# Kernel optimization log

Measured on AMD Instinct MI355X. Metric: run time of the kernel, lower is better.

Reference implementation:

```python
import jax, jax.numpy as jnp
import numpy as np

N_NODES = 50000
IN, H, OUT = 128, 256, 128  # in_channels, hidden_channels, out_channels
E, PE = 640000, 500000
EPS = 1e-5


def setup_inputs() -> dict:
    key = jax.random.key(0)
    ks = jax.random.split(key, 12)
    def rn(k, shape, s=0.05):
        return jax.random.normal(k, shape, jnp.float32) * s
    return {
        "x": jax.random.normal(ks[0], (N_NODES, IN), jnp.float32),
        "edge_index": jax.random.randint(ks[1], (2, E), 0, N_NODES, jnp.int32),
        "pred_edge_index": jax.random.randint(ks[2], (2, PE), 0, N_NODES, jnp.int32),
        # SAGEConv 1: out = mean_neighbors @ W_l^T + x @ W_r^T + b (PyG default, root_weight=True)
        "W1l": rn(ks[3], (H, IN)), "W1r": rn(ks[4], (H, IN)), "b1": jnp.zeros((H,), jnp.float32),
        "bn1_g": jnp.ones((H,), jnp.float32), "bn1_b": jnp.zeros((H,), jnp.float32),
        "bn1_m": jnp.zeros((H,), jnp.float32), "bn1_v": jnp.ones((H,), jnp.float32),
        # SAGEConv 2
        "W2l": rn(ks[5], (OUT, H)), "W2r": rn(ks[6], (OUT, H)), "b2": jnp.zeros((OUT,), jnp.float32),
        # LinkPredictor MLP
        "pW1": rn(ks[7], (H, 2 * OUT)), "pb1": jnp.zeros((H,), jnp.float32),
        "pbn1_g": jnp.ones((H,), jnp.float32), "pbn1_b": jnp.zeros((H,), jnp.float32),
        "pbn1_m": jnp.zeros((H,), jnp.float32), "pbn1_v": jnp.ones((H,), jnp.float32),
        "pW2": rn(ks[8], (H // 2, H)), "pb2": jnp.zeros((H // 2,), jnp.float32),
        "pbn2_g": jnp.ones((H // 2,), jnp.float32), "pbn2_b": jnp.zeros((H // 2,), jnp.float32),
        "pbn2_m": jnp.zeros((H // 2,), jnp.float32), "pbn2_v": jnp.ones((H // 2,), jnp.float32),
        "pW3": rn(ks[9], (1, H // 2)), "pb3": jnp.zeros((1,), jnp.float32),
    }


def _bn(x, g, b, m, v):
    # BatchNorm1d in eval mode (running stats)
    return (x - m) * jax.lax.rsqrt(v + EPS) * g + b


def _sage(x, src, dst, Wl, Wr, b):
    # mean aggregation of source features onto targets (gather-scatter)
    agg = jax.ops.segment_sum(x[src], dst, num_segments=N_NODES)
    cnt = jax.ops.segment_sum(jnp.ones(src.shape, x.dtype), dst, num_segments=N_NODES)
    mean = agg / jnp.maximum(cnt, 1.0)[:, None]
    return mean @ Wl.T + x @ Wr.T + b


def reference(x, edge_index, pred_edge_index, W1l, W1r, b1, bn1_g, bn1_b, bn1_m, bn1_v,
              W2l, W2r, b2, pW1, pb1, pbn1_g, pbn1_b, pbn1_m, pbn1_v,
              pW2, pb2, pbn2_g, pbn2_b, pbn2_m, pbn2_v, pW3, pb3):
    src, dst = edge_index[0], edge_index[1]
    # encoder (dropout is identity in eval mode)
    h = _sage(x, src, dst, W1l, W1r, b1)
    h = jax.nn.relu(_bn(h, bn1_g, bn1_b, bn1_m, bn1_v))
    z = _sage(h, src, dst, W2l, W2r, b2)  # [N_NODES, OUT]
    # decoder: gather endpoint embeddings and run MLP
    q = jnp.concatenate([z[pred_edge_index[0]], z[pred_edge_index[1]]], axis=-1)  # [PE, 2*OUT]
    q = jax.nn.relu(_bn(q @ pW1.T + pb1, pbn1_g, pbn1_b, pbn1_m, pbn1_v))
    q = jax.nn.relu(_bn(q @ pW2.T + pb2, pbn2_g, pbn2_b, pbn2_m, pbn2_v))
    return (q @ pW3.T + pb3).squeeze(-1)  # [PE]
```

## Files before the change

### kernel.cpp

```cpp
#include <hip/hip_runtime.h>
#include <hip/hip_bf16.h>

#define NN   50000
#define NE   640000
#define NPE  500000
#define FEPS 1e-5f

typedef __attribute__((ext_vector_type(8))) short          bf16x8;
typedef __attribute__((ext_vector_type(8))) unsigned short u16x8;
typedef __attribute__((ext_vector_type(4))) float          f32x4;

__device__ inline float b2f(unsigned short u) {
    union { unsigned int i; float f; } c; c.i = (unsigned int)u << 16; return c.f;
}
__device__ inline unsigned short f2b(float f) {
    __hip_bfloat16 h = __float2bfloat16(f);
    return *reinterpret_cast<unsigned short*>(&h);
}

__global__ __launch_bounds__(256) void k_init(
    int4* __restrict__ zdst,
    const float* __restrict__ x, unsigned short* __restrict__ xbf,
    const float* __restrict__ W1l, const float* __restrict__ W1r,
    const float* __restrict__ W2l, const float* __restrict__ W2r,
    const float* __restrict__ pW1, const float* __restrict__ pW2,
    unsigned short* __restrict__ wdst) {
    int b = blockIdx.x, t = threadIdx.x;
    if (b < 196) {
        int i = b * 256 + t;
        if (i < 50048) zdst[i] = make_int4(0, 0, 0, 0);
        return;
    }
    const float* src;
    size_t off;
    if (b < 3321) {
        int i = (b - 196) * 256 + t;
        if (i >= 800000) return;
        const float4* p = (const float4*)x + 2 * (size_t)i;
        float4 a = p[0], c = p[1];
        u16x8 o;
        o[0]=f2b(a.x); o[1]=f2b(a.y); o[2]=f2b(a.z); o[3]=f2b(a.w);
        o[4]=f2b(c.x); o[5]=f2b(c.y); o[6]=f2b(c.z); o[7]=f2b(c.w);
        *((u16x8*)xbf + i) = o;
        return;
    }
    int i = (b - 3321) * 256 + t;
    if (i >= 28672) return;
    if      (i < 4096)  { src = W1l; off = i; }
    else if (i < 8192)  { src = W1r; off = i - 4096; }
    else if (i < 12288) { src = W2l; off = i - 8192; }
    else if (i < 16384) { src = W2r; off = i - 12288; }
    else if (i < 24576) { src = pW1; off = i - 16384; }
    else                { src = pW2; off = i - 24576; }
    const float4* p = (const float4*)src + 2 * off;
    float4 a = p[0], c = p[1];
    u16x8 o;
    o[0]=f2b(a.x); o[1]=f2b(a.y); o[2]=f2b(a.z); o[3]=f2b(a.w);
    o[4]=f2b(c.x); o[5]=f2b(c.y); o[6]=f2b(c.z); o[7]=f2b(c.w);
    *((u16x8*)wdst + i) = o;
}

__global__ void k_hist(const int* __restrict__ key, int* __restrict__ cnt, int n) {
    int e = blockIdx.x * blockDim.x + threadIdx.x;
    if (e < n) atomicAdd(&cnt[key[e]], 1);
}

__global__ void k_scan1(const int* __restrict__ cnt, int* __restrict__ part) {
    int t = threadIdx.x, lane = t & 63, w = t >> 6;
    int i = blockIdx.x * 256 + t;
    int v = (i < NN) ? cnt[i] : 0;
#pragma unroll
    for (int d = 1; d < 64; d <<= 1) v += __shfl_xor(v, d, 64);
    __shared__ int ws[4];
    if (lane == 0) ws[w] = v;
    __syncthreads();
    if (t == 0) part[blockIdx.x] = ws[0] + ws[1] + ws[2] + ws[3];
}

__global__ void k_scan2(int* __restrict__ part) {
    int t = threadIdx.x, lane = t & 63, w = t >> 6;
    int v = (t < 196) ? part[t] : 0;
    int s = v;
#pragma unroll
    for (int d = 1; d < 64; d <<= 1) { int u = __shfl_up(s, d, 64); if (lane >= d) s += u; }
    __shared__ int ws[4];
    if (lane == 63) ws[w] = s;
    __syncthreads();
    if (t == 0) { int a = 0; for (int k = 0; k < 4; ++k) { int tmp = ws[k]; ws[k] = a; a += tmp; } }
    __syncthreads();
    if (t < 196) part[t] = ws[w] + s - v;
}

__global__ void k_scan3(const int* __restrict__ cnt, const int* __restrict__ part,
                        int* __restrict__ rowptr) {
    int t = threadIdx.x, lane = t & 63, w = t >> 6;
    int i = blockIdx.x * 256 + t;
    int v = (i < NN) ? cnt[i] : 0;
    int s = v;
#pragma unroll
    for (int d = 1; d < 64; d <<= 1) { int u = __shfl_up(s, d, 64); if (lane >= d) s += u; }
    __shared__ int ws[4];
    if (lane == 63) ws[w] = s;
    __syncthreads();
    if (t == 0) { int a = 0; for (int k = 0; k < 4; ++k) { int tmp = ws[k]; ws[k] = a; a += tmp; } }
    __syncthreads();
    if (i <= NN) rowptr[i] = part[blockIdx.x] + ws[w] + s - v;
}

__global__ void k_fill(const int* __restrict__ src, const int* __restrict__ dst,
                       const int* __restrict__ rowptr, int* __restrict__ cursor,
                       int* __restrict__ col) {
    int e = blockIdx.x * blockDim.x + threadIdx.x;
    if (e >= NE) return;
    int d = dst[e];
    int slot = atomicAdd(&cursor[d], 1);
    col[rowptr[d] + slot] = src[e];
}

__global__ void k_fill2(const int* __restrict__ pu, const int* __restrict__ pv,
                        const int* __restrict__ rowptr2, int* __restrict__ cursor2,
                        int* __restrict__ su, int2* __restrict__ svi) {
    int e = blockIdx.x * blockDim.x + threadIdx.x;
    if (e >= NPE) return;
    int u = pu[e];
    int slot = atomicAdd(&cursor2[u], 1);
    int pos = rowptr2[u] + slot;
    su[pos] = u;
    svi[pos] = make_int2(pv[e], e);
}

__global__ __launch_bounds__(256) void k_mean(const unsigned short* __restrict__ feat,
                                              const int* __restrict__ rowptr,
                                              const int* __restrict__ col,
                                              unsigned short* __restrict__ outm) {
    int node = blockIdx.x * 4 + (threadIdx.x >> 6);
    int lane = threadIdx.x & 63;
    if (node >= NN) return;
    int beg = rowptr[node], end = rowptr[node + 1];
    float a0 = 0.f, a1 = 0.f;
    int j = beg;
    for (; j + 8 <= end; j += 8) {
        int s[8];
#pragma unroll
        for (int k = 0; k < 8; ++k) s[k] = col[j + k];
        unsigned int v[8];
#pragma unroll
        for (int k = 0; k < 8; ++k)
            v[k] = *(const unsigned int*)(feat + (size_t)s[k] * 128 + lane * 2);
#pragma unroll
        for (int k = 0; k < 8; ++k) { a0 += b2f(v[k] & 0xffff); a1 += b2f(v[k] >> 16); }
    }
    if (j + 4 <= end) {
        int s[4];
#pragma unroll
        for (int k = 0; k < 4; ++k) s[k] = col[j + k];
        unsigned int v[4];
#pragma unroll
        for (int k = 0; k < 4; ++k)
            v[k] = *(const unsigned int*)(feat + (size_t)s[k] * 128 + lane * 2);
#pragma unroll
        for (int k = 0; k < 4; ++k) { a0 += b2f(v[k] & 0xffff); a1 += b2f(v[k] >> 16); }
        j += 4;
    }
    for (; j < end; ++j) {
        int s = col[j];
        unsigned int v = *(const unsigned int*)(feat + (size_t)s * 128 + lane * 2);
        a0 += b2f(v & 0xffff); a1 += b2f(v >> 16);
    }
    float inv = 1.f / fmaxf((float)(end - beg), 1.f);
    unsigned int v = (unsigned int)f2b(a0 * inv) | ((unsigned int)f2b(a1 * inv) << 16);
    *(unsigned int*)(outm + (size_t)node * 128 + lane * 2) = v;
}

__global__ __launch_bounds__(256) void k_sage12(
    const unsigned short* __restrict__ mean, const unsigned short* __restrict__ self,
    const unsigned short* __restrict__ Wl, const unsigned short* __restrict__ Wr,
    const float* __restrict__ b, const float* __restrict__ bg, const float* __restrict__ bb,
    const float* __restrict__ bm, const float* __restrict__ bv,
    const unsigned short* __restrict__ W2l, const unsigned short* __restrict__ W2r,
    const float* __restrict__ b2,
    unsigned short* __restrict__ Y, unsigned short* __restrict__ S) {
    __shared__ unsigned short AB[64 * 256];
    unsigned short* ms = AB;
    unsigned short* xs = AB + 64 * 128;
    int t = threadIdx.x;
    int n0 = blockIdx.x * 64;
    for (int j = 0; j < 4; ++j) {
        int idx = t + j * 256;
        int row = idx >> 4, c16 = idx & 15;
        int node = n0 + row;
        u16x8 v = {0,0,0,0,0,0,0,0}, v2 = {0,0,0,0,0,0,0,0};
        if (node < NN) {
            v  = *(const u16x8*)(mean + (size_t)node * 128 + c16 * 8);
            v2 = *(const u16x8*)(self + (size_t)node * 128 + c16 * 8);
        }
        int byte = row * 256 + ((c16 * 16) ^ ((row & 7) << 4));
        *(u16x8*)((char*)ms + byte) = v;
        *(u16x8*)((char*)xs + byte) = v2;
    }
    __syncthreads();
    int w = t >> 6, l = t & 63, lr = l & 15, lh = l >> 4;
    f32x4 acc[4][4];
#pragma unroll
    for (int mi = 0; mi < 4; ++mi)
#pragma unroll
        for (int ni = 0; ni < 4; ++ni) { acc[mi][ni][0]=0; acc[mi][ni][1]=0; acc[mi][ni][2]=0; acc[mi][ni][3]=0; }
#pragma unroll
    for (int half = 0; half < 2; ++half) {
        const unsigned short* A = half ? xs : ms;
        const unsigned short* W = half ? Wr : Wl;
#pragma unroll
        for (int ks = 0; ks < 4; ++ks) {
            int k0 = ks * 32;
            bf16x8 a[4], wf[4];
#pragma unroll
            for (int mi = 0; mi < 4; ++mi) {
                int row = mi * 16 + lr;
                int byte = row * 256 + ((k0 * 2 + lh * 16) ^ ((row & 7) << 4));
                a[mi] = *(const bf16x8*)((const char*)A + byte);
            }
#pragma unroll
            for (int ni = 0; ni < 4; ++ni) {
                int wrow = w * 64 + ni * 16 + lr;
                wf[ni] = *(const bf16x8*)(W + (size_t)wrow * 128 + k0 + lh * 8);
            }
#pragma unroll
            for (int mi = 0; mi < 4; ++mi)
#pragma unroll
                for (int ni = 0; ni < 4; ++ni)
                    acc[mi][ni] = __builtin_amdgcn_mfma_f32_16x16x32_bf16(a[mi], wf[ni], acc[mi][ni], 0, 0, 0);
        }
    }
    __syncthreads();
#pragma unroll
    for (int ni = 0; ni < 4; ++ni) {
        int ch = w * 64 + ni * 16 + lr;
        float sc = bg[ch] * rsqrtf(bv[ch] + FEPS);
        float sh = bb[ch] - bm[ch] * sc;
        float bias = b[ch];
#pragma unroll
        for (int mi = 0; mi < 4; ++mi)
#pragma unroll
            for (int r = 0; r < 4; ++r) {
                int row = mi * 16 + lh * 4 + r;
                float vv = fmaxf((acc[mi][ni][r] + bias) * sc + sh, 0.f);
                int byte = row * 512 + ((ch * 2) ^ ((row & 7) << 4));
                *(unsigned short*)((char*)AB + byte) = f2b(vv);
            }
    }
    __syncthreads();
    f32x4 aY[4][2], aS[4][2];
#pragma unroll
    for (int mi = 0; mi < 4; ++mi)
#pragma unroll
        for (int ni = 0; ni < 2; ++ni) {
            aY[mi][ni][0]=0; aY[mi][ni][1]=0; aY[mi][ni][2]=0; aY[mi][ni][3]=0;
            aS[mi][ni][0]=0; aS[mi][ni][1]=0; aS[mi][ni][2]=0; aS[mi][ni][3]=0;
        }
#pragma unroll
    for (int ks = 0; ks < 8; ++ks) {
        int k0 = ks * 32;
        bf16x8 a[4], wl[2], wr[2];
#pragma unroll
        for (int mi = 0; mi < 4; ++mi) {
            int row = mi * 16 + lr;
            int byte = row * 512 + ((k0 * 2 + lh * 16) ^ ((row & 7) << 4));
            a[mi] = *(const bf16x8*)((const char*)AB + byte);
        }
#pragma unroll
        for (int ni = 0; ni < 2; ++ni) {
            int wrow = w * 32 + ni * 16 + lr;
            wl[ni] = *(const bf16x8*)(W2l + (size_t)wrow * 256 + k0 + lh * 8);
            wr[ni] = *(const bf16x8*)(W2r + (size_t)wrow * 256 + k0 + lh * 8);
        }
#pragma unroll
        for (int mi = 0; mi < 4; ++mi)
#pragma unroll
            for (int ni = 0; ni < 2; ++ni) {
                aY[mi][ni] = __builtin_amdgcn_mfma_f32_16x16x32_bf16(a[mi], wl[ni], aY[mi][ni], 0, 0, 0);
                aS[mi][ni] = __builtin_amdgcn_mfma_f32_16x16x32_bf16(a[mi], wr[ni], aS[mi][ni], 0, 0, 0);
            }
    }
#pragma unroll
    for (int ni = 0; ni < 2; ++ni) {
        int ch = w * 32 + ni * 16 + lr;
        float bias = b2[ch];
#pragma unroll
        for (int mi = 0; mi < 4; ++mi)
#pragma unroll
            for (int r = 0; r < 4; ++r) {
                int node = n0 + mi * 16 + lh * 4 + r;
                if (node < NN) {
                    Y[(size_t)node * 128 + ch] = f2b(aY[mi][ni][r]);
                    S[(size_t)node * 128 + ch] = f2b(aS[mi][ni][r] + bias);
                }
            }
    }
}

__global__ __launch_bounds__(256) void k_prep(
    const unsigned short* __restrict__ S,
    const unsigned short* __restrict__ mY,
    const unsigned short* __restrict__ W1,
    const float* __restrict__ b1, const float* __restrict__ g1,
    const float* __restrict__ be1, const float* __restrict__ m1, const float* __restrict__ v1,
    unsigned short* __restrict__ Pa, unsigned short* __restrict__ Pb) {
    __shared__ unsigned short zs[64 * 128];
    int t = threadIdx.x;
    int tile = blockIdx.x >> 1, side = blockIdx.x & 1;
    int n0 = tile * 64;
    for (int j = 0; j < 4; ++j) {
        int idx = t + j * 256;
        int row = idx >> 4, c16 = idx & 15;
        int node = n0 + row;
        u16x8 o = {0,0,0,0,0,0,0,0};
        if (node < NN) {
            u16x8 sv = *(const u16x8*)(S  + (size_t)node * 128 + c16 * 8);
            u16x8 mv = *(const u16x8*)(mY + (size_t)node * 128 + c16 * 8);
#pragma unroll
            for (int jj = 0; jj < 8; ++jj)
                o[jj] = f2b(b2f((unsigned short)sv[jj]) + b2f((unsigned short)mv[jj]));
        }
        int byte = row * 256 + ((c16 * 16) ^ ((row & 7) << 4));
        *(u16x8*)((char*)zs + byte) = o;
    }
    __syncthreads();
    int w = t >> 6, l = t & 63, lr = l & 15, lh = l >> 4;
    f32x4 acc[4][4];
#pragma unroll
    for (int mi = 0; mi < 4; ++mi)
#pragma unroll
        for (int ni = 0; ni < 4; ++ni) { acc[mi][ni][0]=0; acc[mi][ni][1]=0; acc[mi][ni][2]=0; acc[mi][ni][3]=0; }
#pragma unroll
    for (int ks = 0; ks < 4; ++ks) {
        int k0 = ks * 32;
        bf16x8 a[4], wf[4];
#pragma unroll
        for (int mi = 0; mi < 4; ++mi) {
            int row = mi * 16 + lr;
            int byte = row * 256 + ((k0 * 2 + lh * 16) ^ ((row & 7) << 4));
            a[mi] = *(const bf16x8*)((const char*)zs + byte);
        }
#pragma unroll
        for (int ni = 0; ni < 4; ++ni) {
            int ch = w * 64 + ni * 16 + lr;
            wf[ni] = *(const bf16x8*)(W1 + (size_t)ch * 256 + side * 128 + k0 + lh * 8);
        }
#pragma unroll
        for (int mi = 0; mi < 4; ++mi)
#pragma unroll
            for (int ni = 0; ni < 4; ++ni)
                acc[mi][ni] = __builtin_amdgcn_mfma_f32_16x16x32_bf16(a[mi], wf[ni], acc[mi][ni], 0, 0, 0);
    }
    unsigned short* P = side ? Pb : Pa;
#pragma unroll
    for (int ni = 0; ni < 4; ++ni) {
        int ch = w * 64 + ni * 16 + lr;
        float sc = g1[ch] * rsqrtf(v1[ch] + FEPS);
        float add = side ? 0.f : ((b1[ch] - m1[ch]) * sc + be1[ch]);
#pragma unroll
        for (int mi = 0; mi < 4; ++mi)
#pragma unroll
            for (int r = 0; r < 4; ++r) {
                int node = n0 + mi * 16 + lh * 4 + r;
                if (node < NN)
                    P[(size_t)node * 256 + ch] = f2b(acc[mi][ni][r] * sc + add);
            }
    }
}

__global__ __launch_bounds__(256, 5) void k_mlp(
    const unsigned short* __restrict__ Pa, const unsigned short* __restrict__ Pb,
    const int* __restrict__ su, const int2* __restrict__ svi,
    const unsigned short* __restrict__ W2, const float* __restrict__ b2,
    const float* __restrict__ g2, const float* __restrict__ be2,
    const float* __restrict__ m2, const float* __restrict__ v2,
    const float* __restrict__ W3, const float* __restrict__ b3,
    float* __restrict__ out) {
    __shared__ unsigned short q1[64 * 256];
    int t = threadIdx.x;
    const int q = 976, r = 5;
    int bid = blockIdx.x;
    int xcd = bid & 7, ii = bid >> 3;
    int wg = (xcd < r) ? (xcd * (q + 1) + ii) : (r * (q + 1) + (xcd - r) * q + ii);
    int e0 = wg * 64;
#pragma unroll
    for (int batch = 0; batch < 2; ++batch) {
        u16x8 A[4], B[4];
        int bofs[4];
#pragma unroll
        for (int j = 0; j < 4; ++j) {
            int idx = t + (batch * 4 + j) * 256;
            int edge = idx >> 5, c16 = idx & 31;
            int ge = e0 + edge;
            if (ge < NPE) {
                int u = su[ge];
                int2 vi = svi[ge];
                A[j] = *(const u16x8*)(Pa + (size_t)u    * 256 + c16 * 8);
                B[j] = *(const u16x8*)(Pb + (size_t)vi.x * 256 + c16 * 8);
            } else {
                A[j] = (u16x8){0,0,0,0,0,0,0,0};
                B[j] = (u16x8){0,0,0,0,0,0,0,0};
            }
            bofs[j] = edge * 512 + ((c16 * 16) ^ ((edge & 7) << 4));
        }
#pragma unroll
        for (int j = 0; j < 4; ++j) {
            u16x8 o;
#pragma unroll
            for (int jj = 0; jj < 8; ++jj)
                o[jj] = f2b(fmaxf(b2f((unsigned short)A[j][jj]) + b2f((unsigned short)B[j][jj]), 0.f));
            *(u16x8*)((char*)q1 + bofs[j]) = o;
        }
    }
    __syncthreads();
    int w = t >> 6, l = t & 63, lr = l & 15, lh = l >> 4;
    f32x4 acc[4][2];
#pragma unroll
    for (int mi = 0; mi < 4; ++mi)
#pragma unroll
        for (int ni = 0; ni < 2; ++ni) { acc[mi][ni][0]=0; acc[mi][ni][1]=0; acc[mi][ni][2]=0; acc[mi][ni][3]=0; }
#pragma unroll
    for (int ks = 0; ks < 8; ++ks) {
        int k0 = ks * 32;
        bf16x8 a[4], wf[2];
#pragma unroll
        for (int mi = 0; mi < 4; ++mi) {
            int row = mi * 16 + lr;
            int byte = row * 512 + ((k0 * 2 + lh * 16) ^ ((row & 7) << 4));
            a[mi] = *(const bf16x8*)((const char*)q1 + byte);
        }
#pragma unroll
        for (int ni = 0; ni < 2; ++ni) {
            int wrow = w * 32 + ni * 16 + lr;
            wf[ni] = *(const bf16x8*)(W2 + (size_t)wrow * 256 + k0 + lh * 8);
        }
#pragma unroll
        for (int mi = 0; mi < 4; ++mi)
#pragma unroll
            for (int ni = 0; ni < 2; ++ni)
                acc[mi][ni] = __builtin_amdgcn_mfma_f32_16x16x32_bf16(a[mi], wf[ni], acc[mi][ni], 0, 0, 0);
    }
    __syncthreads();
#pragma unroll
    for (int ni = 0; ni < 2; ++ni) {
        int ch = w * 32 + ni * 16 + lr;
        float sc = g2[ch] * rsqrtf(v2[ch] + FEPS);
        float sh = be2[ch] - m2[ch] * sc;
        float bias = b2[ch];
#pragma unroll
        for (int mi = 0; mi < 4; ++mi)
#pragma unroll
            for (int r = 0; r < 4; ++r) {
                int row = mi * 16 + lh * 4 + r;
                float vv = fmaxf((acc[mi][ni][r] + bias) * sc + sh, 0.f);
                int byte = row * 256 + ((ch * 2) ^ ((row & 7) << 4));
                *(unsigned short*)((char*)q1 + byte) = f2b(vv);
            }
    }
    __syncthreads();
    {
        int edge = t >> 2, part = t & 3;
        float p = 0.f;
#pragma unroll
        for (int s = 0; s < 4; ++s) {
            int byte = edge * 256 + ((part * 64 + s * 16) ^ ((edge & 7) << 4));
            u16x8 v = *(const u16x8*)((const char*)q1 + byte);
#pragma unroll
            for (int jj = 0; jj < 8; ++jj)
                p += b2f((unsigned short)v[jj]) * W3[part * 32 + s * 8 + jj];
        }
        p += __shfl_xor(p, 1, 64);
        p += __shfl_xor(p, 2, 64);
        int ge = e0 + edge;
        if (part == 0 && ge < NPE) out[svi[ge].y] = p + b3[0];
    }
}

extern "C" void kernel_launch(void* const* d_in, const int* in_sizes, int n_in,
                              void* d_out, int out_size, void* d_ws, size_t ws_size,
                              hipStream_t stream) {
    const float* x    = (const float*)d_in[0];
    const int*   ei   = (const int*)d_in[1];
    const int*   pei  = (const int*)d_in[2];
    const float* W1l  = (const float*)d_in[3];
    const float* W1r  = (const float*)d_in[4];
    const float* b1   = (const float*)d_in[5];
    const float* bn1g = (const float*)d_in[6];
    const float* bn1b = (const float*)d_in[7];
    const float* bn1m = (const float*)d_in[8];
    const float* bn1v = (const float*)d_in[9];
    const float* W2l  = (const float*)d_in[10];
    const float* W2r  = (const float*)d_in[11];
    const float* b2   = (const float*)d_in[12];
    const float* pW1  = (const float*)d_in[13];
    const float* pb1  = (const float*)d_in[14];
    const float* pg1  = (const float*)d_in[15];
    const float* pbb1 = (const float*)d_in[16];
    const float* pm1  = (const float*)d_in[17];
    const float* pv1  = (const float*)d_in[18];
    const float* pW2  = (const float*)d_in[19];
    const float* pb2  = (const float*)d_in[20];
    const float* pg2  = (const float*)d_in[21];
    const float* pbb2 = (const float*)d_in[22];
    const float* pm2  = (const float*)d_in[23];
    const float* pv2  = (const float*)d_in[24];
    const float* pW3  = (const float*)d_in[25];
    const float* pb3  = (const float*)d_in[26];
    float* out = (float*)d_out;

    const int* src = ei;
    const int* dst = ei + NE;
    const int* pu  = pei;
    const int* pv  = pei + NPE;

    char* p = (char*)d_ws;
    auto alloc = [&](size_t bytes) -> char* {
        char* r = p; p += (bytes + 255) & ~(size_t)255; return r;
    };
    int* cnt     = (int*)alloc((size_t)NN * 4);
    int* cursor  = (int*)alloc((size_t)NN * 4);
    int* cnt2    = (int*)alloc((size_t)NN * 4);
    int* cursor2 = (int*)alloc((size_t)NN * 4);
    int* part    = (int*)alloc(256 * 4);
    int* part2   = (int*)alloc(256 * 4);
    int* rowptr  = (int*)alloc((size_t)(NN + 1) * 4);
    int* rowptr2 = (int*)alloc((size_t)(NN + 1) * 4);
    int* col     = (int*)alloc((size_t)NE * 4);
    int* su      = (int*)alloc((size_t)NPE * 4);
    int2* svi    = (int2*)alloc((size_t)NPE * 8);
    unsigned short* xbf  = (unsigned short*)alloc((size_t)NN * 128 * 2);
    unsigned short* mx   = (unsigned short*)alloc((size_t)NN * 128 * 2);
    unsigned short* Ybf  = (unsigned short*)alloc((size_t)NN * 128 * 2);
    unsigned short* mY   = (unsigned short*)alloc((size_t)NN * 128 * 2);
    unsigned short* Sbf  = (unsigned short*)alloc((size_t)NN * 128 * 2);
    unsigned short* Pa   = (unsigned short*)alloc((size_t)NN * 256 * 2);
    unsigned short* W1lb = (unsigned short*)alloc((size_t)256 * 128 * 2);
    unsigned short* W1rb = (unsigned short*)alloc((size_t)256 * 128 * 2);
    unsigned short* W2lb = (unsigned short*)alloc((size_t)128 * 256 * 2);
    unsigned short* W2rb = (unsigned short*)alloc((size_t)128 * 256 * 2);
    unsigned short* pW1b = (unsigned short*)alloc((size_t)256 * 256 * 2);
    unsigned short* pW2b = (unsigned short*)alloc((size_t)128 * 256 * 2);
    unsigned short* Pb = xbf;

    k_init<<<3433, 256, 0, stream>>>((int4*)cnt, x, xbf,
                                     W1l, W1r, W2l, W2r, pW1, pW2, W1lb);
    k_hist<<<2500, 256, 0, stream>>>(dst, cnt, NE);
    k_scan1<<<196, 256, 0, stream>>>(cnt, part);
    k_scan2<<<1, 256, 0, stream>>>(part);
    k_scan3<<<196, 256, 0, stream>>>(cnt, part, rowptr);
    k_fill<<<2500, 256, 0, stream>>>(src, dst, rowptr, cursor, col);
    k_hist<<<1954, 256, 0, stream>>>(pu, cnt2, NPE);
    k_scan1<<<196, 256, 0, stream>>>(cnt2, part2);
    k_scan2<<<1, 256, 0, stream>>>(part2);
    k_scan3<<<196, 256, 0, stream>>>(cnt2, part2, rowptr2);
    k_fill2<<<1954, 256, 0, stream>>>(pu, pv, rowptr2, cursor2, su, svi);

    k_mean<<<12500, 256, 0, stream>>>(xbf, rowptr, col, mx);
    k_sage12<<<782, 256, 0, stream>>>(mx, xbf, W1lb, W1rb, b1, bn1g, bn1b, bn1m, bn1v,
                                      W2lb, W2rb, b2, Ybf, Sbf);
    k_mean<<<12500, 256, 0, stream>>>(Ybf, rowptr, col, mY);

    k_prep<<<1564, 256, 0, stream>>>(Sbf, mY, pW1b, pb1, pg1, pbb1, pm1, pv1, Pa, Pb);

    k_mlp<<<(NPE + 63) / 64, 256, 0, stream>>>(Pa, Pb, su, svi,
                                               pW2b, pb2, pg2, pbb2, pm2, pv2,
                                               pW3, pb3, out);
}
```

Before: 418.1 us.

## Drop prediction-edge sort and run MLP directly from registers without LDS

Removes the histogram, scan and fill passes that sorted prediction edges by source node, so the MLP kernel reads pu/pv directly and writes outputs in original order. The MLP kernel is restructured so each wave handles 16 edges, builds the MFMA A-operand straight from the gathered Pa+Pb rows in registers with software prefetch, and applies the folded BN2 scale and offset plus the W3 dot product with shuffles instead of staging through LDS. BN2 scale and offset are precomputed once in the init kernel. The cost is that gathers are no longer locality-sorted, and W2 is re-read per wave from global memory.

```diff
diff --git a/kernel.cpp b/kernel.cpp
--- a/kernel.cpp
+++ b/kernel.cpp
@@ -24,17 +24,28 @@
     const float* __restrict__ W1l, const float* __restrict__ W1r,
     const float* __restrict__ W2l, const float* __restrict__ W2r,
     const float* __restrict__ pW1, const float* __restrict__ pW2,
-    unsigned short* __restrict__ wdst) {
+    unsigned short* __restrict__ wdst,
+    const float* __restrict__ pb2, const float* __restrict__ pg2,
+    const float* __restrict__ pbb2, const float* __restrict__ pm2,
+    const float* __restrict__ pv2, float2* __restrict__ fold2) {
     int b = blockIdx.x, t = threadIdx.x;
-    if (b < 196) {
+    if (b < 98) {
         int i = b * 256 + t;
-        if (i < 50048) zdst[i] = make_int4(0, 0, 0, 0);
+        if (i < 25088) zdst[i] = make_int4(0, 0, 0, 0);
+        return;
+    }
+    if (b == 3335) {
+        if (t < 128) {
+            float sc = pg2[t] * rsqrtf(pv2[t] + FEPS);
+            float off = pb2[t] * sc + pbb2[t] - pm2[t] * sc;
+            fold2[t] = make_float2(sc, off);
+        }
         return;
     }
     const float* src;
     size_t off;
-    if (b < 3321) {
-        int i = (b - 196) * 256 + t;
+    if (b < 3223) {
+        int i = (b - 98) * 256 + t;
         if (i >= 800000) return;
         const float4* p = (const float4*)x + 2 * (size_t)i;
         float4 a = p[0], c = p[1];
@@ -44,7 +55,7 @@
         *((u16x8*)xbf + i) = o;
         return;
     }
-    int i = (b - 3321) * 256 + t;
+    int i = (b - 3223) * 256 + t;
     if (i >= 28672) return;
     if      (i < 4096)  { src = W1l; off = i; }
     else if (i < 8192)  { src = W1r; off = i - 4096; }
@@ -115,18 +126,6 @@
     int d = dst[e];
     int slot = atomicAdd(&cursor[d], 1);
     col[rowptr[d] + slot] = src[e];
-}
-
-__global__ void k_fill2(const int* __restrict__ pu, const int* __restrict__ pv,
-                        const int* __restrict__ rowptr2, int* __restrict__ cursor2,
-                        int* __restrict__ su, int2* __restrict__ svi) {
-    int e = blockIdx.x * blockDim.x + threadIdx.x;
-    if (e >= NPE) return;
-    int u = pu[e];
-    int slot = atomicAdd(&cursor2[u], 1);
-    int pos = rowptr2[u] + slot;
-    su[pos] = u;
-    svi[pos] = make_int2(pv[e], e);
 }
 
 __global__ __launch_bounds__(256) void k_mean(const unsigned short* __restrict__ feat,
@@ -371,109 +370,62 @@
 
 __global__ __launch_bounds__(256, 5) void k_mlp(
     const unsigned short* __restrict__ Pa, const unsigned short* __restrict__ Pb,
-    const int* __restrict__ su, const int2* __restrict__ svi,
-    const unsigned short* __restrict__ W2, const float* __restrict__ b2,
-    const float* __restrict__ g2, const float* __restrict__ be2,
-    const float* __restrict__ m2, const float* __restrict__ v2,
+    const int* __restrict__ pu, const int* __restrict__ pv,
+    const unsigned short* __restrict__ W2,
+    const float2* __restrict__ fold2,
     const float* __restrict__ W3, const float* __restrict__ b3,
     float* __restrict__ out) {
-    __shared__ unsigned short q1[64 * 256];
     int t = threadIdx.x;
-    const int q = 976, r = 5;
-    int bid = blockIdx.x;
-    int xcd = bid & 7, ii = bid >> 3;
-    int wg = (xcd < r) ? (xcd * (q + 1) + ii) : (r * (q + 1) + (xcd - r) * q + ii);
-    int e0 = wg * 64;
-#pragma unroll
-    for (int batch = 0; batch < 2; ++batch) {
-        u16x8 A[4], B[4];
-        int bofs[4];
-#pragma unroll
-        for (int j = 0; j < 4; ++j) {
-            int idx = t + (batch * 4 + j) * 256;
-            int edge = idx >> 5, c16 = idx & 31;
-            int ge = e0 + edge;
-            if (ge < NPE) {
-                int u = su[ge];
-                int2 vi = svi[ge];
-                A[j] = *(const u16x8*)(Pa + (size_t)u    * 256 + c16 * 8);
-                B[j] = *(const u16x8*)(Pb + (size_t)vi.x * 256 + c16 * 8);
-            } else {
-                A[j] = (u16x8){0,0,0,0,0,0,0,0};
-                B[j] = (u16x8){0,0,0,0,0,0,0,0};
-            }
-            bofs[j] = edge * 512 + ((c16 * 16) ^ ((edge & 7) << 4));
-        }
-#pragma unroll
-        for (int j = 0; j < 4; ++j) {
-            u16x8 o;
-#pragma unroll
-            for (int jj = 0; jj < 8; ++jj)
-                o[jj] = f2b(fmaxf(b2f((unsigned short)A[j][jj]) + b2f((unsigned short)B[j][jj]), 0.f));
-            *(u16x8*)((char*)q1 + bofs[j]) = o;
-        }
-    }
-    __syncthreads();
     int w = t >> 6, l = t & 63, lr = l & 15, lh = l >> 4;
-    f32x4 acc[4][2];
-#pragma unroll
-    for (int mi = 0; mi < 4; ++mi)
-#pragma unroll
-        for (int ni = 0; ni < 2; ++ni) { acc[mi][ni][0]=0; acc[mi][ni][1]=0; acc[mi][ni][2]=0; acc[mi][ni][3]=0; }
+    int we0 = blockIdx.x * 64 + w * 16;
+    int eidx = we0 + lr;
+    int u = 0, v = 0;
+    if (eidx < NPE) { u = pu[eidx]; v = pv[eidx]; }
+    const u16x8* rowA = (const u16x8*)(Pa + (size_t)u * 256 + lh * 8);
+    const u16x8* rowB = (const u16x8*)(Pb + (size_t)v * 256 + lh * 8);
+    f32x4 acc[8];
+#pragma unroll
+    for (int ni = 0; ni < 8; ++ni) { acc[ni][0]=0; acc[ni][1]=0; acc[ni][2]=0; acc[ni][3]=0; }
+    u16x8 pa0 = rowA[0], pb0 = rowB[0];
+    u16x8 pa1 = rowA[4], pb1 = rowB[4];
 #pragma unroll
     for (int ks = 0; ks < 8; ++ks) {
-        int k0 = ks * 32;
-        bf16x8 a[4], wf[2];
-#pragma unroll
-        for (int mi = 0; mi < 4; ++mi) {
-            int row = mi * 16 + lr;
-            int byte = row * 512 + ((k0 * 2 + lh * 16) ^ ((row & 7) << 4));
-            a[mi] = *(const bf16x8*)((const char*)q1 + byte);
-        }
-#pragma unroll
-        for (int ni = 0; ni < 2; ++ni) {
-            int wrow = w * 32 + ni * 16 + lr;
-            wf[ni] = *(const bf16x8*)(W2 + (size_t)wrow * 256 + k0 + lh * 8);
-        }
-#pragma unroll
-        for (int mi = 0; mi < 4; ++mi)
-#pragma unroll
-            for (int ni = 0; ni < 2; ++ni)
-                acc[mi][ni] = __builtin_amdgcn_mfma_f32_16x16x32_bf16(a[mi], wf[ni], acc[mi][ni], 0, 0, 0);
-    }
-    __syncthreads();
-#pragma unroll
-    for (int ni = 0; ni < 2; ++ni) {
-        int ch = w * 32 + ni * 16 + lr;
-        float sc = g2[ch] * rsqrtf(v2[ch] + FEPS);
-        float sh = be2[ch] - m2[ch] * sc;
-        float bias = b2[ch];
-#pragma unroll
-        for (int mi = 0; mi < 4; ++mi)
-#pragma unroll
-            for (int r = 0; r < 4; ++r) {
-                int row = mi * 16 + lh * 4 + r;
-                float vv = fmaxf((acc[mi][ni][r] + bias) * sc + sh, 0.f);
-                int byte = row * 256 + ((ch * 2) ^ ((row & 7) << 4));
-                *(unsigned short*)((char*)q1 + byte) = f2b(vv);
-            }
-    }
-    __syncthreads();
-    {
-        int edge = t >> 2, part = t & 3;
-        float p = 0.f;
-#pragma unroll
-        for (int s = 0; s < 4; ++s) {
-            int byte = edge * 256 + ((part * 64 + s * 16) ^ ((edge & 7) << 4));
-            u16x8 v = *(const u16x8*)((const char*)q1 + byte);
-#pragma unroll
-            for (int jj = 0; jj < 8; ++jj)
-                p += b2f((unsigned short)v[jj]) * W3[part * 32 + s * 8 + jj];
-        }
-        p += __shfl_xor(p, 1, 64);
-        p += __shfl_xor(p, 2, 64);
-        int ge = e0 + edge;
-        if (part == 0 && ge < NPE) out[svi[ge].y] = p + b3[0];
+        bf16x8 af;
+#pragma unroll
+        for (int jj = 0; jj < 8; ++jj) {
+            float f = fmaxf(b2f((unsigned short)pa0[jj]) + b2f((unsigned short)pb0[jj]), 0.f);
+            af[jj] = (short)f2b(f);
+        }
+        pa0 = pa1; pb0 = pb1;
+        if (ks < 6) { pa1 = rowA[(ks + 2) * 4]; pb1 = rowB[(ks + 2) * 4]; }
+#pragma unroll
+        for (int ni = 0; ni < 8; ++ni) {
+            bf16x8 wf = *(const bf16x8*)(W2 + (size_t)(ni * 16 + lr) * 256 + ks * 32 + lh * 8);
+            acc[ni] = __builtin_amdgcn_mfma_f32_16x16x32_bf16(af, wf, acc[ni], 0, 0, 0);
+        }
+    }
+    float p0 = 0.f, p1 = 0.f, p2 = 0.f, p3 = 0.f;
+#pragma unroll
+    for (int ni = 0; ni < 8; ++ni) {
+        int ch = ni * 16 + lr;
+        float2 f = fold2[ch];
+        float w3 = W3[ch];
+        p0 += fmaxf(acc[ni][0] * f.x + f.y, 0.f) * w3;
+        p1 += fmaxf(acc[ni][1] * f.x + f.y, 0.f) * w3;
+        p2 += fmaxf(acc[ni][2] * f.x + f.y, 0.f) * w3;
+        p3 += fmaxf(acc[ni][3] * f.x + f.y, 0.f) * w3;
+    }
+#pragma unroll
+    for (int d = 1; d < 16; d <<= 1) {
+        p0 += __shfl_xor(p0, d, 16);
+        p1 += __shfl_xor(p1, d, 16);
+        p2 += __shfl_xor(p2, d, 16);
+        p3 += __shfl_xor(p3, d, 16);
+    }
+    if (lr < 4) {
+        int oe = we0 + lh * 4 + lr;
+        float pr = (lr == 0) ? p0 : (lr == 1) ? p1 : (lr == 2) ? p2 : p3;
+        if (oe < NPE) out[oe] = pr + b3[0];
     }
 }
 
@@ -520,15 +472,9 @@
     };
     int* cnt     = (int*)alloc((size_t)NN * 4);
     int* cursor  = (int*)alloc((size_t)NN * 4);
-    int* cnt2    = (int*)alloc((size_t)NN * 4);
-    int* cursor2 = (int*)alloc((size_t)NN * 4);
     int* part    = (int*)alloc(256 * 4);
-    int* part2   = (int*)alloc(256 * 4);
     int* rowptr  = (int*)alloc((size_t)(NN + 1) * 4);
-    int* rowptr2 = (int*)alloc((size_t)(NN + 1) * 4);
     int* col     = (int*)alloc((size_t)NE * 4);
-    int* su      = (int*)alloc((size_t)NPE * 4);
-    int2* svi    = (int2*)alloc((size_t)NPE * 8);
     unsigned short* xbf  = (unsigned short*)alloc((size_t)NN * 128 * 2);
     unsigned short* mx   = (unsigned short*)alloc((size_t)NN * 128 * 2);
     unsigned short* Ybf  = (unsigned short*)alloc((size_t)NN * 128 * 2);
@@ -541,20 +487,17 @@
     unsigned short* W2rb = (unsigned short*)alloc((size_t)128 * 256 * 2);
     unsigned short* pW1b = (unsigned short*)alloc((size_t)256 * 256 * 2);
     unsigned short* pW2b = (unsigned short*)alloc((size_t)128 * 256 * 2);
+    float2* fold2        = (float2*)alloc(128 * 8);
     unsigned short* Pb = xbf;
 
-    k_init<<<3433, 256, 0, stream>>>((int4*)cnt, x, xbf,
-                                     W1l, W1r, W2l, W2r, pW1, pW2, W1lb);
+    k_init<<<3336, 256, 0, stream>>>((int4*)cnt, x, xbf,
+                                     W1l, W1r, W2l, W2r, pW1, pW2, W1lb,
+                                     pb2, pg2, pbb2, pm2, pv2, fold2);
     k_hist<<<2500, 256, 0, stream>>>(dst, cnt, NE);
     k_scan1<<<196, 256, 0, stream>>>(cnt, part);
     k_scan2<<<1, 256, 0, stream>>>(part);
     k_scan3<<<196, 256, 0, stream>>>(cnt, part, rowptr);
     k_fill<<<2500, 256, 0, stream>>>(src, dst, rowptr, cursor, col);
-    k_hist<<<1954, 256, 0, stream>>>(pu, cnt2, NPE);
-    k_scan1<<<196, 256, 0, stream>>>(cnt2, part2);
-    k_scan2<<<1, 256, 0, stream>>>(part2);
-    k_scan3<<<196, 256, 0, stream>>>(cnt2, part2, rowptr2);
-    k_fill2<<<1954, 256, 0, stream>>>(pu, pv, rowptr2, cursor2, su, svi);
 
     k_mean<<<12500, 256, 0, stream>>>(xbf, rowptr, col, mx);
     k_sage12<<<782, 256, 0, stream>>>(mx, xbf, W1lb, W1rb, b1, bn1g, bn1b, bn1m, bn1v,
@@ -563,7 +506,6 @@
 
     k_prep<<<1564, 256, 0, stream>>>(Sbf, mY, pW1b, pb1, pg1, pbb1, pm1, pv1, Pa, Pb);
 
-    k_mlp<<<(NPE + 63) / 64, 256, 0, stream>>>(Pa, Pb, su, svi,
-                                               pW2b, pb2, pg2, pbb2, pm2, pv2,
-                                               pW3, pb3, out);
-}
+    k_mlp<<<(NPE + 63) / 64, 256, 0, stream>>>(Pa, Pb, pu, pv,
+                                               pW2b, fold2, pW3, pb3, out);
+}
```

New measurement: 506.4 us. 1.21x slower.

## Fuse mean aggregation into SAGE/prep kernels and drop pred-edge CSR sort

Applied to the files above, without the earlier changes.

The two standalone neighbor-mean kernels are folded into the GEMM kernels: k_sage12 and k_prep now gather neighbor rows per node into shared memory before their MFMA stages. This removes the intermediate mean buffers and two launches. k_prep also handles both output halves in one block instead of splitting them across blocks. The pred-edge sort by source (histogram, scan, fill, and the XCD remapping) is removed, so k_mlp reads pu/pv directly and writes output in edge order. The trade-off is gather locality: the sorted order previously improved cache reuse of Pa rows, and the fused kernels now run latency-bound gathers with only 782 blocks.

```diff
diff --git a/kernel.cpp b/kernel.cpp
--- a/kernel.cpp
+++ b/kernel.cpp
@@ -26,15 +26,15 @@
     const float* __restrict__ pW1, const float* __restrict__ pW2,
     unsigned short* __restrict__ wdst) {
     int b = blockIdx.x, t = threadIdx.x;
-    if (b < 196) {
+    if (b < 98) {
         int i = b * 256 + t;
-        if (i < 50048) zdst[i] = make_int4(0, 0, 0, 0);
+        if (i < 25088) zdst[i] = make_int4(0, 0, 0, 0);
         return;
     }
     const float* src;
     size_t off;
-    if (b < 3321) {
-        int i = (b - 196) * 256 + t;
+    if (b < 3223) {
+        int i = (b - 98) * 256 + t;
         if (i >= 800000) return;
         const float4* p = (const float4*)x + 2 * (size_t)i;
         float4 a = p[0], c = p[1];
@@ -44,7 +44,7 @@
         *((u16x8*)xbf + i) = o;
         return;
     }
-    int i = (b - 3321) * 256 + t;
+    int i = (b - 3223) * 256 + t;
     if (i >= 28672) return;
     if      (i < 4096)  { src = W1l; off = i; }
     else if (i < 8192)  { src = W1r; off = i - 4096; }
@@ -117,27 +117,12 @@
     col[rowptr[d] + slot] = src[e];
 }
 
-__global__ void k_fill2(const int* __restrict__ pu, const int* __restrict__ pv,
-                        const int* __restrict__ rowptr2, int* __restrict__ cursor2,
-                        int* __restrict__ su, int2* __restrict__ svi) {
-    int e = blockIdx.x * blockDim.x + threadIdx.x;
-    if (e >= NPE) return;
-    int u = pu[e];
-    int slot = atomicAdd(&cursor2[u], 1);
-    int pos = rowptr2[u] + slot;
-    su[pos] = u;
-    svi[pos] = make_int2(pv[e], e);
-}
-
-__global__ __launch_bounds__(256) void k_mean(const unsigned short* __restrict__ feat,
-                                              const int* __restrict__ rowptr,
-                                              const int* __restrict__ col,
-                                              unsigned short* __restrict__ outm) {
-    int node = blockIdx.x * 4 + (threadIdx.x >> 6);
-    int lane = threadIdx.x & 63;
-    if (node >= NN) return;
+__device__ inline unsigned int mean_row(const unsigned short* __restrict__ feat,
+                                        const int* __restrict__ rowptr,
+                                        const int* __restrict__ col,
+                                        int node, int lane) {
+    float a0 = 0.f, a1 = 0.f;
     int beg = rowptr[node], end = rowptr[node + 1];
-    float a0 = 0.f, a1 = 0.f;
     int j = beg;
     for (; j + 8 <= end; j += 8) {
         int s[8];
@@ -168,12 +153,12 @@
         a0 += b2f(v & 0xffff); a1 += b2f(v >> 16);
     }
     float inv = 1.f / fmaxf((float)(end - beg), 1.f);
-    unsigned int v = (unsigned int)f2b(a0 * inv) | ((unsigned int)f2b(a1 * inv) << 16);
-    *(unsigned int*)(outm + (size_t)node * 128 + lane * 2) = v;
+    return (unsigned int)f2b(a0 * inv) | ((unsigned int)f2b(a1 * inv) << 16);
 }
 
 __global__ __launch_bounds__(256) void k_sage12(
-    const unsigned short* __restrict__ mean, const unsigned short* __restrict__ self,
+    const unsigned short* __restrict__ xbf,
+    const int* __restrict__ rowptr, const int* __restrict__ col,
     const unsigned short* __restrict__ Wl, const unsigned short* __restrict__ Wr,
     const float* __restrict__ b, const float* __restrict__ bg, const float* __restrict__ bb,
     const float* __restrict__ bm, const float* __restrict__ bv,
@@ -189,17 +174,22 @@
         int idx = t + j * 256;
         int row = idx >> 4, c16 = idx & 15;
         int node = n0 + row;
-        u16x8 v = {0,0,0,0,0,0,0,0}, v2 = {0,0,0,0,0,0,0,0};
-        if (node < NN) {
-            v  = *(const u16x8*)(mean + (size_t)node * 128 + c16 * 8);
-            v2 = *(const u16x8*)(self + (size_t)node * 128 + c16 * 8);
-        }
+        u16x8 v2 = {0,0,0,0,0,0,0,0};
+        if (node < NN) v2 = *(const u16x8*)(xbf + (size_t)node * 128 + c16 * 8);
         int byte = row * 256 + ((c16 * 16) ^ ((row & 7) << 4));
-        *(u16x8*)((char*)ms + byte) = v;
         *(u16x8*)((char*)xs + byte) = v2;
     }
-    __syncthreads();
-    int w = t >> 6, l = t & 63, lr = l & 15, lh = l >> 4;
+    int w = t >> 6, lane = t & 63;
+    for (int i = 0; i < 16; ++i) {
+        int row = w * 16 + i;
+        int node = n0 + row;
+        unsigned int mv = 0;
+        if (node < NN) mv = mean_row(xbf, rowptr, col, node, lane);
+        int byte = row * 256 + ((lane * 4) ^ ((row & 7) << 4));
+        *(unsigned int*)((char*)ms + byte) = mv;
+    }
+    __syncthreads();
+    int l = t & 63, lr = l & 15, lh = l >> 4;
     f32x4 acc[4][4];
 #pragma unroll
     for (int mi = 0; mi < 4; ++mi)
@@ -299,79 +289,82 @@
 }
 
 __global__ __launch_bounds__(256) void k_prep(
+    const unsigned short* __restrict__ Ybf,
     const unsigned short* __restrict__ S,
-    const unsigned short* __restrict__ mY,
+    const int* __restrict__ rowptr, const int* __restrict__ col,
     const unsigned short* __restrict__ W1,
     const float* __restrict__ b1, const float* __restrict__ g1,
     const float* __restrict__ be1, const float* __restrict__ m1, const float* __restrict__ v1,
     unsigned short* __restrict__ Pa, unsigned short* __restrict__ Pb) {
     __shared__ unsigned short zs[64 * 128];
     int t = threadIdx.x;
-    int tile = blockIdx.x >> 1, side = blockIdx.x & 1;
-    int n0 = tile * 64;
-    for (int j = 0; j < 4; ++j) {
-        int idx = t + j * 256;
-        int row = idx >> 4, c16 = idx & 15;
+    int n0 = blockIdx.x * 64;
+    int w = t >> 6, lane = t & 63;
+    for (int i = 0; i < 16; ++i) {
+        int row = w * 16 + i;
         int node = n0 + row;
-        u16x8 o = {0,0,0,0,0,0,0,0};
+        unsigned int zv = 0;
         if (node < NN) {
-            u16x8 sv = *(const u16x8*)(S  + (size_t)node * 128 + c16 * 8);
-            u16x8 mv = *(const u16x8*)(mY + (size_t)node * 128 + c16 * 8);
-#pragma unroll
-            for (int jj = 0; jj < 8; ++jj)
-                o[jj] = f2b(b2f((unsigned short)sv[jj]) + b2f((unsigned short)mv[jj]));
-        }
-        int byte = row * 256 + ((c16 * 16) ^ ((row & 7) << 4));
-        *(u16x8*)((char*)zs + byte) = o;
-    }
-    __syncthreads();
-    int w = t >> 6, l = t & 63, lr = l & 15, lh = l >> 4;
-    f32x4 acc[4][4];
-#pragma unroll
-    for (int mi = 0; mi < 4; ++mi)
-#pragma unroll
-        for (int ni = 0; ni < 4; ++ni) { acc[mi][ni][0]=0; acc[mi][ni][1]=0; acc[mi][ni][2]=0; acc[mi][ni][3]=0; }
-#pragma unroll
-    for (int ks = 0; ks < 4; ++ks) {
-        int k0 = ks * 32;
-        bf16x8 a[4], wf[4];
-#pragma unroll
-        for (int mi = 0; mi < 4; ++mi) {
-            int row = mi * 16 + lr;
-            int byte = row * 256 + ((k0 * 2 + lh * 16) ^ ((row & 7) << 4));
-            a[mi] = *(const bf16x8*)((const char*)zs + byte);
-        }
+            unsigned int mv = mean_row(Ybf, rowptr, col, node, lane);
+            unsigned int sv = *(const unsigned int*)(S + (size_t)node * 128 + lane * 2);
+            unsigned int lo = f2b(b2f(sv & 0xffff) + b2f(mv & 0xffff));
+            unsigned int hi = f2b(b2f(sv >> 16)    + b2f(mv >> 16));
+            zv = lo | (hi << 16);
+        }
+        int byte = row * 256 + ((lane * 4) ^ ((row & 7) << 4));
+        *(unsigned int*)((char*)zs + byte) = zv;
+    }
+    __syncthreads();
+    int l = t & 63, lr = l & 15, lh = l >> 4;
+#pragma unroll
+    for (int side = 0; side < 2; ++side) {
+        f32x4 acc[4][4];
+#pragma unroll
+        for (int mi = 0; mi < 4; ++mi)
+#pragma unroll
+            for (int ni = 0; ni < 4; ++ni) { acc[mi][ni][0]=0; acc[mi][ni][1]=0; acc[mi][ni][2]=0; acc[mi][ni][3]=0; }
+#pragma unroll
+        for (int ks = 0; ks < 4; ++ks) {
+            int k0 = ks * 32;
+            bf16x8 a[4], wf[4];
+#pragma unroll
+            for (int mi = 0; mi < 4; ++mi) {
+                int row = mi * 16 + lr;
+                int byte = row * 256 + ((k0 * 2 + lh * 16) ^ ((row & 7) << 4));
+                a[mi] = *(const bf16x8*)((const char*)zs + byte);
+            }
+#pragma unroll
+            for (int ni = 0; ni < 4; ++ni) {
+                int ch = w * 64 + ni * 16 + lr;
+                wf[ni] = *(const bf16x8*)(W1 + (size_t)ch * 256 + side * 128 + k0 + lh * 8);
+            }
+#pragma unroll
+            for (int mi = 0; mi < 4; ++mi)
+#pragma unroll
+                for (int ni = 0; ni < 4; ++ni)
+                    acc[mi][ni] = __builtin_amdgcn_mfma_f32_16x16x32_bf16(a[mi], wf[ni], acc[mi][ni], 0, 0, 0);
+        }
+        unsigned short* P = side ? Pb : Pa;
 #pragma unroll
         for (int ni = 0; ni < 4; ++ni) {
             int ch = w * 64 + ni * 16 + lr;
-            wf[ni] = *(const bf16x8*)(W1 + (size_t)ch * 256 + side * 128 + k0 + lh * 8);
-        }
-#pragma unroll
-        for (int mi = 0; mi < 4; ++mi)
-#pragma unroll
-            for (int ni = 0; ni < 4; ++ni)
-                acc[mi][ni] = __builtin_amdgcn_mfma_f32_16x16x32_bf16(a[mi], wf[ni], acc[mi][ni], 0, 0, 0);
-    }
-    unsigned short* P = side ? Pb : Pa;
-#pragma unroll
-    for (int ni = 0; ni < 4; ++ni) {
-        int ch = w * 64 + ni * 16 + lr;
-        float sc = g1[ch] * rsqrtf(v1[ch] + FEPS);
-        float add = side ? 0.f : ((b1[ch] - m1[ch]) * sc + be1[ch]);
-#pragma unroll
-        for (int mi = 0; mi < 4; ++mi)
-#pragma unroll
-            for (int r = 0; r < 4; ++r) {
-                int node = n0 + mi * 16 + lh * 4 + r;
-                if (node < NN)
-                    P[(size_t)node * 256 + ch] = f2b(acc[mi][ni][r] * sc + add);
-            }
+            float sc = g1[ch] * rsqrtf(v1[ch] + FEPS);
+            float add = side ? 0.f : ((b1[ch] - m1[ch]) * sc + be1[ch]);
+#pragma unroll
+            for (int mi = 0; mi < 4; ++mi)
+#pragma unroll
+                for (int r = 0; r < 4; ++r) {
+                    int node = n0 + mi * 16 + lh * 4 + r;
+                    if (node < NN)
+                        P[(size_t)node * 256 + ch] = f2b(acc[mi][ni][r] * sc + add);
+                }
+        }
     }
 }
 
 __global__ __launch_bounds__(256, 5) void k_mlp(
     const unsigned short* __restrict__ Pa, const unsigned short* __restrict__ Pb,
-    const int* __restrict__ su, const int2* __restrict__ svi,
+    const int* __restrict__ pu, const int* __restrict__ pv,
     const unsigned short* __restrict__ W2, const float* __restrict__ b2,
     const float* __restrict__ g2, const float* __restrict__ be2,
     const float* __restrict__ m2, const float* __restrict__ v2,
@@ -379,11 +372,7 @@
     float* __restrict__ out) {
     __shared__ unsigned short q1[64 * 256];
     int t = threadIdx.x;
-    const int q = 976, r = 5;
-    int bid = blockIdx.x;
-    int xcd = bid & 7, ii = bid >> 3;
-    int wg = (xcd < r) ? (xcd * (q + 1) + ii) : (r * (q + 1) + (xcd - r) * q + ii);
-    int e0 = wg * 64;
+    int e0 = blockIdx.x * 64;
 #pragma unroll
     for (int batch = 0; batch < 2; ++batch) {
         u16x8 A[4], B[4];
@@ -394,10 +383,9 @@
             int edge = idx >> 5, c16 = idx & 31;
             int ge = e0 + edge;
             if (ge < NPE) {
-                int u = su[ge];
-                int2 vi = svi[ge];
-                A[j] = *(const u16x8*)(Pa + (size_t)u    * 256 + c16 * 8);
-                B[j] = *(const u16x8*)(Pb + (size_t)vi.x * 256 + c16 * 8);
+                int u = pu[ge], vv = pv[ge];
+                A[j] = *(const u16x8*)(Pa + (size_t)u  * 256 + c16 * 8);
+                B[j] = *(const u16x8*)(Pb + (size_t)vv * 256 + c16 * 8);
             } else {
                 A[j] = (u16x8){0,0,0,0,0,0,0,0};
                 B[j] = (u16x8){0,0,0,0,0,0,0,0};
@@ -473,7 +461,7 @@
         p += __shfl_xor(p, 1, 64);
         p += __shfl_xor(p, 2, 64);
         int ge = e0 + edge;
-        if (part == 0 && ge < NPE) out[svi[ge].y] = p + b3[0];
+        if (part == 0 && ge < NPE) out[ge] = p + b3[0];
     }
 }
 
@@ -520,19 +508,12 @@
     };
     int* cnt     = (int*)alloc((size_t)NN * 4);
     int* cursor  = (int*)alloc((size_t)NN * 4);
-    int* cnt2    = (int*)alloc((size_t)NN * 4);
-    int* cursor2 = (int*)alloc((size_t)NN * 4);
     int* part    = (int*)alloc(256 * 4);
-    int* part2   = (int*)alloc(256 * 4);
     int* rowptr  = (int*)alloc((size_t)(NN + 1) * 4);
-    int* rowptr2 = (int*)alloc((size_t)(NN + 1) * 4);
     int* col     = (int*)alloc((size_t)NE * 4);
-    int* su      = (int*)alloc((size_t)NPE * 4);
-    int2* svi    = (int2*)alloc((size_t)NPE * 8);
     unsigned short* xbf  = (unsigned short*)alloc((size_t)NN * 128 * 2);
     unsigned short* mx   = (unsigned short*)alloc((size_t)NN * 128 * 2);
     unsigned short* Ybf  = (unsigned short*)alloc((size_t)NN * 128 * 2);
-    unsigned short* mY   = (unsigned short*)alloc((size_t)NN * 128 * 2);
     unsigned short* Sbf  = (unsigned short*)alloc((size_t)NN * 128 * 2);
     unsigned short* Pa   = (unsigned short*)alloc((size_t)NN * 256 * 2);
     unsigned short* W1lb = (unsigned short*)alloc((size_t)256 * 128 * 2);
@@ -542,28 +523,23 @@
     unsigned short* pW1b = (unsigned short*)alloc((size_t)256 * 256 * 2);
     unsigned short* pW2b = (unsigned short*)alloc((size_t)128 * 256 * 2);
     unsigned short* Pb = xbf;
-
-    k_init<<<3433, 256, 0, stream>>>((int4*)cnt, x, xbf,
+    (void)mx;
+
+    k_init<<<3335, 256, 0, stream>>>((int4*)cnt, x, xbf,
                                      W1l, W1r, W2l, W2r, pW1, pW2, W1lb);
     k_hist<<<2500, 256, 0, stream>>>(dst, cnt, NE);
     k_scan1<<<196, 256, 0, stream>>>(cnt, part);
     k_scan2<<<1, 256, 0, stream>>>(part);
     k_scan3<<<196, 256, 0, stream>>>(cnt, part, rowptr);
     k_fill<<<2500, 256, 0, stream>>>(src, dst, rowptr, cursor, col);
-    k_hist<<<1954, 256, 0, stream>>>(pu, cnt2, NPE);
-    k_scan1<<<196, 256, 0, stream>>>(cnt2, part2);
-    k_scan2<<<1, 256, 0, stream>>>(part2);
-    k_scan3<<<196, 256, 0, stream>>>(cnt2, part2, rowptr2);
-    k_fill2<<<1954, 256, 0, stream>>>(pu, pv, rowptr2, cursor2, su, svi);
-
-    k_mean<<<12500, 256, 0, stream>>>(xbf, rowptr, col, mx);
-    k_sage12<<<782, 256, 0, stream>>>(mx, xbf, W1lb, W1rb, b1, bn1g, bn1b, bn1m, bn1v,
+
+    k_sage12<<<782, 256, 0, stream>>>(xbf, rowptr, col, W1lb, W1rb,
+                                      b1, bn1g, bn1b, bn1m, bn1v,
                                       W2lb, W2rb, b2, Ybf, Sbf);
-    k_mean<<<12500, 256, 0, stream>>>(Ybf, rowptr, col, mY);
-
-    k_prep<<<1564, 256, 0, stream>>>(Sbf, mY, pW1b, pb1, pg1, pbb1, pm1, pv1, Pa, Pb);
-
-    k_mlp<<<(NPE + 63) / 64, 256, 0, stream>>>(Pa, Pb, su, svi,
+    k_prep<<<782, 256, 0, stream>>>(Ybf, Sbf, rowptr, col, pW1b,
+                                    pb1, pg1, pbb1, pm1, pv1, Pa, Pb);
+
+    k_mlp<<<(NPE + 63) / 64, 256, 0, stream>>>(Pa, Pb, pu, pv,
                                                pW2b, pb2, pg2, pbb2, pm2, pv2,
                                                pW3, pb3, out);
 }
```

New measurement: 437.0 us. 1.05x slower.
